# Kernel optimization log

Measured on AMD Instinct MI355X. Metric: run time of the kernel, lower is better.

Reference implementation:

```python
import jax, jax.numpy as jnp
import numpy as np

NU, NI = 100000, 50000
N = NU + NI
CU, CI = 100, 100
D = 64
NL = 3
NNZ = 4_000_000
CNNZ = 5000
B = 4096


def setup_inputs() -> dict:
    key = jax.random.key(0)
    ks = jax.random.split(key, 24)
    def edges(k1, k2, k3, nnz, n):
        return (jax.random.randint(k1, (nnz,), 0, n, dtype=jnp.int32),
                jax.random.randint(k2, (nnz,), 0, n, dtype=jnp.int32),
                jax.random.uniform(k3, (nnz,), dtype=jnp.float32) * 0.05)
    ar, ac, av = edges(ks[0], ks[1], ks[2], NNZ, N)
    s1r, s1c, s1v = edges(ks[3], ks[4], ks[5], NNZ, N)
    s2r, s2c, s2v = edges(ks[6], ks[7], ks[8], NNZ, N)
    cr, cc, cv = edges(ks[9], ks[10], ks[11], CNNZ, CU + CI)
    return {
        "user_emb": jax.random.normal(ks[12], (NU, D), dtype=jnp.float32) * 0.1,
        "item_emb": jax.random.normal(ks[13], (NI, D), dtype=jnp.float32) * 0.1,
        "adj_rows": ar, "adj_cols": ac, "adj_vals": av,
        "sg1_rows": s1r, "sg1_cols": s1c, "sg1_vals": s1v,
        "sg2_rows": s2r, "sg2_cols": s2c, "sg2_vals": s2v,
        "uc": jax.random.uniform(ks[14], (NU, CU), dtype=jnp.float32),
        "ic": jax.random.uniform(ks[15], (NI, CI), dtype=jnp.float32),
        "cg_rows": cr, "cg_cols": cc, "cg_vals": cv,
        "users": jax.random.randint(ks[16], (B,), 0, NU, dtype=jnp.int32),
        "items": jax.random.randint(ks[17], (B,), 0, NI, dtype=jnp.int32),
        "neg_items": jax.random.randint(ks[18], (B,), 0, NI, dtype=jnp.int32),
    }


def _gcn(rows, cols, vals, ego, n):
    """n_layers of SpMM propagation + mean over layer outputs (incl. layer 0)."""
    acc = ego
    x = ego
    for _ in range(NL):
        x = jax.ops.segment_sum(vals[:, None] * x[cols], rows, num_segments=n)
        acc = acc + x
    return acc / (NL + 1)


def reference(user_emb, item_emb,
              adj_rows, adj_cols, adj_vals,
              sg1_rows, sg1_cols, sg1_vals,
              sg2_rows, sg2_cols, sg2_vals,
              uc, ic, cg_rows, cg_cols, cg_vals,
              users, items, neg_items):
    ego = jnp.concatenate([user_emb, item_emb], axis=0)  # [N, D]
    e0 = _gcn(adj_rows, adj_cols, adj_vals, ego, N)
    e1 = _gcn(sg1_rows, sg1_cols, sg1_vals, ego, N)
    e2 = _gcn(sg2_rows, sg2_cols, sg2_vals, ego, N)
    # community GCN: project node embeddings onto community space, propagate, lift back
    ucf = uc.T @ user_emb                                # [CU, D]
    icf = ic.T @ item_emb                                # [CI, D]
    ec = _gcn(cg_rows, cg_cols, cg_vals,
              jnp.concatenate([ucf, icf], axis=0), CU + CI)
    u3 = uc @ ec[:CU]                                    # [NU, D]
    i3 = ic @ ec[CU:]                                    # [NI, D]
    user_f = jnp.concatenate([e0[:NU], e1[:NU], e2[:NU], u3], axis=1)  # [NU, 4D]
    item_f = jnp.concatenate([e0[NU:], e1[NU:], e2[NU:], i3], axis=1)  # [NI, 4D]
    ue = user_f[users]
    ie = item_f[items]
    ne = item_f[neg_items]
    # sup_logits = <u, i_pos> - <u, i_neg>
    return jnp.sum(ue * (ie - ne), axis=-1)
```

## Files before the change

kernel.cpp:

```cpp
#include <hip/hip_runtime.h>
#include <hip/hip_fp16.h>
#include <cstdint>
#include <cstddef>

#define NU_ 100000
#define NI_ 50000
#define NN_ 150000
#define D_  64
#define NNZ_ 4000000
#define CN_ 200
#define CNNZ_ 5000
#define B_ 4096

#define NB2   512
#define RPB2  293
#define SLICE 40
#define NBLK  512
#define ECAP  8448

#define PROJB 1024

#define VSC_   256.0f
#define IVSC_  (1.0f / 256.0f)

#if defined(__has_builtin)
#if __has_builtin(__builtin_amdgcn_cvt_scalef32_pk_f32_fp4) && \
    __has_builtin(__builtin_amdgcn_cvt_scalef32_pk_fp4_f32)
#define USE_FP4 1
#endif
#endif
#ifndef USE_FP4
#define USE_FP4 0
#endif

#if USE_FP4
#define FSC0 8.0f
#define FSC1 32.0f
#define FSC2 512.0f
#define ROWB 32
#else
#define FSC0 32.0f
#define FSC1 32.0f
#define FSC2 32.0f
#define ROWB 64
#endif

typedef float v2f __attribute__((ext_vector_type(2)));
typedef int   v4i __attribute__((ext_vector_type(4)));
typedef float v4f __attribute__((ext_vector_type(4)));

__device__ __forceinline__ float cv8(unsigned char b) {
    return __builtin_amdgcn_cvt_f32_fp8((int)b, 0);
}


#if USE_FP4
__global__ __launch_bounds__(256) void k_toq(const float* __restrict__ a,
                                             const float* __restrict__ b,
                                             unsigned* __restrict__ dst) {
    size_t gid = (size_t)blockIdx.x * 256 + threadIdx.x;
    size_t off = gid * 8;
    if (off >= (size_t)NN_ * D_) return;
    const float* src = (off < (size_t)NU_ * D_) ? a + off : b + (off - (size_t)NU_ * D_);
    float4 f0 = *(const float4*)src;
    float4 f1 = *(const float4*)(src + 4);
    unsigned w = 0;
    w = __builtin_amdgcn_cvt_scalef32_pk_fp4_f32(w, f0.x * FSC0, f0.y * FSC0, 1.0f, 0);
    w = __builtin_amdgcn_cvt_scalef32_pk_fp4_f32(w, f0.z * FSC0, f0.w * FSC0, 1.0f, 1);
    w = __builtin_amdgcn_cvt_scalef32_pk_fp4_f32(w, f1.x * FSC0, f1.y * FSC0, 1.0f, 2);
    w = __builtin_amdgcn_cvt_scalef32_pk_fp4_f32(w, f1.z * FSC0, f1.w * FSC0, 1.0f, 3);
    dst[gid] = w;
}
#else
__global__ __launch_bounds__(256) void k_toq(const float* __restrict__ a,
                                             const float* __restrict__ b,
                                             unsigned* __restrict__ dst) {
    size_t gid = (size_t)blockIdx.x * 256 + threadIdx.x;
    size_t off = gid * 4;
    if (off >= (size_t)NN_ * D_) return;
    const float* src = (off < (size_t)NU_ * D_) ? a + off : b + (off - (size_t)NU_ * D_);
    float4 f = *(const float4*)src;
    int p = 0;
    p = __builtin_amdgcn_cvt_pk_fp8_f32(f.x * FSC0, f.y * FSC0, p, false);
    p = __builtin_amdgcn_cvt_pk_fp8_f32(f.z * FSC0, f.w * FSC0, p, true);
    dst[gid] = (unsigned)p;
}
#endif


__global__ __launch_bounds__(256) void k_bin(const int* __restrict__ rows,
                                             const int* __restrict__ cols,
                                             const float* __restrict__ vals,
                                             int* __restrict__ bcnt,
                                             int2* __restrict__ gbuf) {
    __shared__ int lcur[NB2];
    int t = threadIdx.x;
    for (int i = t; i < NB2; i += 256) lcur[i] = 0;
    __syncthreads();
    size_t blockbase = (size_t)blockIdx.x * NB2 * SLICE;

    for (int base = blockIdx.x * 1024; base < NNZ_; base += gridDim.x * 1024) {
        int i0 = base + t * 4;
        if (i0 < NNZ_) {
            v4i r4 = __builtin_nontemporal_load((const v4i*)(rows + i0));
            v4i c4 = __builtin_nontemporal_load((const v4i*)(cols + i0));
            v4f v4 = __builtin_nontemporal_load((const v4f*)(vals + i0));
            #pragma unroll
            for (int k = 0; k < 4; k++) {
                int r = (k == 0) ? r4.x : (k == 1) ? r4.y : (k == 2) ? r4.z : r4.w;
                int c = (k == 0) ? c4.x : (k == 1) ? c4.y : (k == 2) ? c4.z : c4.w;
                float v = (k == 0) ? v4.x : (k == 1) ? v4.y : (k == 2) ? v4.z : v4.w;
                int b  = r / RPB2;
                int rl = r - b * RPB2;
                int pos = atomicAdd(&lcur[b], 1);
                if (pos < SLICE)
                    gbuf[blockbase + (size_t)b * SLICE + pos] =
                        make_int2((rl << 18) | c, __float_as_int(v));
            }
        }
    }
    __syncthreads();
    for (int i = t; i < NB2; i += 256)
        bcnt[(size_t)blockIdx.x * NB2 + i] = min(lcur[i], SLICE);
}


__global__ void k_btot(const int* __restrict__ bcnt, int* __restrict__ btot) {
    __shared__ int s[256];
    int b = blockIdx.x, t = threadIdx.x;
    int sum = 0;
    for (int sl = t; sl < NBLK; sl += 256) sum += bcnt[(size_t)sl * NB2 + b];
    s[t] = sum;
    __syncthreads();
    for (int o = 128; o > 0; o >>= 1) {
        if (t < o) s[t] += s[t + o];
        __syncthreads();
    }
    if (t == 0) btot[b] = s[0];
}

__global__ void k_bscan(const int* __restrict__ btot, int* __restrict__ bbase,
                        int* __restrict__ row_ptr) {
    __shared__ int s[NB2];
    int t = threadIdx.x;
    int v = btot[t];
    s[t] = v;
    __syncthreads();
    for (int o = 1; o < NB2; o <<= 1) {
        int x = (t >= o) ? s[t - o] : 0;
        __syncthreads();
        s[t] += x;
        __syncthreads();
    }
    bbase[t] = s[t] - v;
    if (t == NB2 - 1) row_ptr[NN_] = s[t];
}


__global__ __launch_bounds__(1024) void k_csr(const int* __restrict__ bcnt,
                                              const int2* __restrict__ gbuf,
                                              const int* __restrict__ bbase,
                                              const int* __restrict__ btot,
                                              int* __restrict__ row_ptr,
                                              unsigned* __restrict__ ep) {
    __shared__ int h[RPB2];
    __shared__ int hx[RPB2];
    __shared__ unsigned estage[ECAP];
    int b = blockIdx.x, t = threadIdx.x;
    for (int i = t; i < RPB2; i += 1024) h[i] = 0;
    __syncthreads();

    int sl = t >> 1, part = t & 1;
    int n = bcnt[(size_t)sl * NB2 + b];
    const int2* src = gbuf + ((size_t)sl * NB2 + b) * SLICE;

    for (int i = part; i < n; i += 2) {
        unsigned xv = *(const unsigned*)(src + i);
        atomicAdd(&h[xv >> 18], 1);
    }
    __syncthreads();

    if (t < RPB2) hx[t] = h[t];
    __syncthreads();
    for (int o = 1; o < RPB2; o <<= 1) {
        int x = 0;
        if (t < RPB2 && t >= o) x = hx[t - o];
        __syncthreads();
        if (t < RPB2) hx[t] += x;
        __syncthreads();
    }

    int base = bbase[b];
    int r0 = b * RPB2;
    if (t < RPB2) {
        int excl = hx[t] - h[t];
        if (r0 + t < NN_) row_ptr[r0 + t] = base + excl;
        h[t] = excl;
    }
    __syncthreads();

    for (int i = part; i < n; i += 2) {
        int2 e = src[i];
        unsigned ex = (unsigned)e.x;
        int rl = ex >> 18;
        unsigned c = ex & 0x3FFFFu;
        float v = __int_as_float(e.y) * VSC_;
        unsigned v8 = (unsigned)__builtin_amdgcn_cvt_pk_fp8_f32(v, 0.f, 0, false) & 0xFFu;
        int pos = atomicAdd(&h[rl], 1);
        if (pos < ECAP) estage[pos] = c | (v8 << 24);
    }
    __syncthreads();

    int total = btot[b];
    if (total > ECAP) total = ECAP;
    for (int i = t; i < total; i += 1024) ep[base + i] = estage[i];
}


__global__ __launch_bounds__(256) void k_spmm(const int* __restrict__ rp,
                                              const unsigned* __restrict__ ep,
                                              const unsigned char* __restrict__ xq,
                                              float invs, float outsc,
                                              unsigned char* __restrict__ xn) {
    int w = (blockIdx.x * 256 + threadIdx.x) >> 6;
    if (w >= NN_) return;
    int lane = threadIdx.x & 63;
    int oct = lane >> 3;
    int l8  = lane & 7;
    int j0 = rp[w], j1 = rp[w + 1];
    v2f a01 = {0.f, 0.f}, a23 = {0.f, 0.f}, a45 = {0.f, 0.f}, a67 = {0.f, 0.f};
    #pragma unroll 2
    for (int j = j0; j < j1; j += 8) {
        int je = j + oct;
        unsigned e = (je < j1) ? ep[je] : 0u;
        float v = __builtin_amdgcn_cvt_f32_fp8((int)e, 3) * invs;
        v2f vv = {v, v};
#if USE_FP4
        unsigned raw = *(const unsigned*)(xq + (size_t)(e & 0x3FFFFu) * 32 + l8 * 4);
        a01 += vv * __builtin_amdgcn_cvt_scalef32_pk_f32_fp4(raw, 1.0f, 0);
        a23 += vv * __builtin_amdgcn_cvt_scalef32_pk_f32_fp4(raw, 1.0f, 1);
        a45 += vv * __builtin_amdgcn_cvt_scalef32_pk_f32_fp4(raw, 1.0f, 2);
        a67 += vv * __builtin_amdgcn_cvt_scalef32_pk_f32_fp4(raw, 1.0f, 3);
#else
        uint2 raw = *(const uint2*)(xq + (size_t)(e & 0x3FFFFu) * 64 + l8 * 8);
        a01 += vv * __builtin_amdgcn_cvt_pk_f32_fp8((int)raw.x, false);
        a23 += vv * __builtin_amdgcn_cvt_pk_f32_fp8((int)raw.x, true);
        a45 += vv * __builtin_amdgcn_cvt_pk_f32_fp8((int)raw.y, false);
        a67 += vv * __builtin_amdgcn_cvt_pk_f32_fp8((int)raw.y, true);
#endif
    }
    float d0 = a01[0], d1 = a01[1], d2 = a23[0], d3 = a23[1];
    float d4 = a45[0], d5 = a45[1], d6 = a67[0], d7 = a67[1];
    #pragma unroll
    for (int o = 32; o >= 8; o >>= 1) {
        d0 += __shfl_xor(d0, o, 64); d1 += __shfl_xor(d1, o, 64);
        d2 += __shfl_xor(d2, o, 64); d3 += __shfl_xor(d3, o, 64);
        d4 += __shfl_xor(d4, o, 64); d5 += __shfl_xor(d5, o, 64);
        d6 += __shfl_xor(d6, o, 64); d7 += __shfl_xor(d7, o, 64);
    }
    if (lane < 8) {
#if USE_FP4
        unsigned o2 = 0;
        o2 = __builtin_amdgcn_cvt_scalef32_pk_fp4_f32(o2, d0 * outsc, d1 * outsc, 1.0f, 0);
        o2 = __builtin_amdgcn_cvt_scalef32_pk_fp4_f32(o2, d2 * outsc, d3 * outsc, 1.0f, 1);
        o2 = __builtin_amdgcn_cvt_scalef32_pk_fp4_f32(o2, d4 * outsc, d5 * outsc, 1.0f, 2);
        o2 = __builtin_amdgcn_cvt_scalef32_pk_fp4_f32(o2, d6 * outsc, d7 * outsc, 1.0f, 3);
        *(unsigned*)(xn + (size_t)w * 32 + l8 * 4) = o2;
#else
        int p0 = 0, p1 = 0;
        p0 = __builtin_amdgcn_cvt_pk_fp8_f32(d0 * outsc, d1 * outsc, p0, false);
        p0 = __builtin_amdgcn_cvt_pk_fp8_f32(d2 * outsc, d3 * outsc, p0, true);
        p1 = __builtin_amdgcn_cvt_pk_fp8_f32(d4 * outsc, d5 * outsc, p1, false);
        p1 = __builtin_amdgcn_cvt_pk_fp8_f32(d6 * outsc, d7 * outsc, p1, true);
        uint2 o2; o2.x = (unsigned)p0; o2.y = (unsigned)p1;
        *(uint2*)(xn + (size_t)w * 64 + l8 * 8) = o2;
#endif
    }
}


__global__ __launch_bounds__(256) void k_spmm_s(const int* __restrict__ rp,
                                                const unsigned* __restrict__ ep,
                                                const unsigned char* __restrict__ xq,
                                                float invs,
                                                const int* __restrict__ users,
                                                const int* __restrict__ items,
                                                const int* __restrict__ negs,
                                                float* __restrict__ x3s) {
    int s = (blockIdx.x * 256 + threadIdx.x) >> 6;
    if (s >= 3 * B_) return;
    int lane = threadIdx.x & 63;
    int oct = lane >> 3;
    int l8  = lane & 7;
    int node;
    if (s < B_)          node = users[s];
    else if (s < 2 * B_) node = NU_ + items[s - B_];
    else                 node = NU_ + negs[s - 2 * B_];
    int j0 = rp[node], j1 = rp[node + 1];
    v2f a01 = {0.f, 0.f}, a23 = {0.f, 0.f}, a45 = {0.f, 0.f}, a67 = {0.f, 0.f};
    #pragma unroll 2
    for (int j = j0; j < j1; j += 8) {
        int je = j + oct;
        unsigned e = (je < j1) ? ep[je] : 0u;
        float v = __builtin_amdgcn_cvt_f32_fp8((int)e, 3) * invs;
        v2f vv = {v, v};
#if USE_FP4
        unsigned raw = *(const unsigned*)(xq + (size_t)(e & 0x3FFFFu) * 32 + l8 * 4);
        a01 += vv * __builtin_amdgcn_cvt_scalef32_pk_f32_fp4(raw, 1.0f, 0);
        a23 += vv * __builtin_amdgcn_cvt_scalef32_pk_f32_fp4(raw, 1.0f, 1);
        a45 += vv * __builtin_amdgcn_cvt_scalef32_pk_f32_fp4(raw, 1.0f, 2);
        a67 += vv * __builtin_amdgcn_cvt_scalef32_pk_f32_fp4(raw, 1.0f, 3);
#else
        uint2 raw = *(const uint2*)(xq + (size_t)(e & 0x3FFFFu) * 64 + l8 * 8);
        a01 += vv * __builtin_amdgcn_cvt_pk_f32_fp8((int)raw.x, false);
        a23 += vv * __builtin_amdgcn_cvt_pk_f32_fp8((int)raw.x, true);
        a45 += vv * __builtin_amdgcn_cvt_pk_f32_fp8((int)raw.y, false);
        a67 += vv * __builtin_amdgcn_cvt_pk_f32_fp8((int)raw.y, true);
#endif
    }
    float d0 = a01[0], d1 = a01[1], d2 = a23[0], d3 = a23[1];
    float d4 = a45[0], d5 = a45[1], d6 = a67[0], d7 = a67[1];
    #pragma unroll
    for (int o = 32; o >= 8; o >>= 1) {
        d0 += __shfl_xor(d0, o, 64); d1 += __shfl_xor(d1, o, 64);
        d2 += __shfl_xor(d2, o, 64); d3 += __shfl_xor(d3, o, 64);
        d4 += __shfl_xor(d4, o, 64); d5 += __shfl_xor(d5, o, 64);
        d6 += __shfl_xor(d6, o, 64); d7 += __shfl_xor(d7, o, 64);
    }
    if (lane < 8) {
        float* dst = x3s + (size_t)s * D_ + l8 * 8;
        *(float4*)dst       = make_float4(d0, d1, d2, d3);
        *(float4*)(dst + 4) = make_float4(d4, d5, d6, d7);
    }
}


__device__ __forceinline__ float ldq(const unsigned char* x, size_t row, int lane, float inv) {
#if USE_FP4
    unsigned byte = x[row * 32 + (lane >> 1)];
    v2f pr = __builtin_amdgcn_cvt_scalef32_pk_f32_fp4(byte, 1.0f, 0);
    return ((lane & 1) ? pr[1] : pr[0]) * inv;
#else
    return cv8(x[row * 64 + lane]) * inv;
#endif
}

template<bool FIRST>
__global__ void k_dot_graph(const float* __restrict__ ue, const float* __restrict__ ie,
                            const unsigned char* __restrict__ x1,
                            const unsigned char* __restrict__ x2,
                            const float* __restrict__ x3s,
                            const int* __restrict__ users, const int* __restrict__ items,
                            const int* __restrict__ negs, float* __restrict__ out) {
    int w = (blockIdx.x * blockDim.x + threadIdx.x) >> 6;
    int lane = threadIdx.x & 63;
    if (w >= B_) return;
    int u = users[w], ip = items[w], in_ = negs[w];
    const float i1 = 1.0f / FSC1, i2 = 1.0f / FSC2;
    size_t ru = (size_t)u, ri = (size_t)(NU_ + ip), rn = (size_t)(NU_ + in_);
    float du = ue[(size_t)u * D_ + lane]
             + ldq(x1, ru, lane, i1) + ldq(x2, ru, lane, i2) + x3s[(size_t)w * D_ + lane];
    float di = ie[(size_t)ip * D_ + lane]
             + ldq(x1, ri, lane, i1) + ldq(x2, ri, lane, i2) + x3s[(size_t)(B_ + w) * D_ + lane];
    float dn = ie[(size_t)in_ * D_ + lane]
             + ldq(x1, rn, lane, i1) + ldq(x2, rn, lane, i2) + x3s[(size_t)(2 * B_ + w) * D_ + lane];
    float p = du * (di - dn);
    for (int o = 32; o > 0; o >>= 1) p += __shfl_xor(p, o, 64);
    if (lane == 0) {
        if (FIRST) out[w] = p * 0.0625f;
        else       out[w] += p * 0.0625f;
    }
}


__global__ __launch_bounds__(256) void k_proj(const float* __restrict__ mat,
                                              const float* __restrict__ emb,
                                              int n, float* __restrict__ pbuf) {
    __shared__ float se[8 * 64];
    __shared__ float sc[8 * 100];
    int t = threadIdx.x;
    int d = t & 63, c0 = t >> 6;
    float a[25];
    #pragma unroll
    for (int k = 0; k < 25; k++) a[k] = 0.f;

    int upb = (n + gridDim.x - 1) / gridDim.x;
    int u0 = blockIdx.x * upb;
    int u1 = min(u0 + upb, n);
    int ub = u0;
    for (; ub + 8 <= u1; ub += 8) {
        const float4* e4 = (const float4*)(emb + (size_t)ub * 64);
        const float4* c4 = (const float4*)(mat + (size_t)ub * 100);
        float4* se4 = (float4*)se;
        float4* sc4 = (float4*)sc;
        for (int idx = t; idx < 328; idx += 256) {
            if (idx < 128) se4[idx] = e4[idx];
            else           sc4[idx - 128] = c4[idx - 128];
        }
        __syncthreads();
        #pragma unroll
        for (int ul = 0; ul < 8; ++ul) {
            float ev = se[(ul << 6) + d];
            #pragma unroll
            for (int k = 0; k < 25; k++)
                a[k] += sc[ul * 100 + c0 + (k << 2)] * ev;
        }
        __syncthreads();
    }
    if (ub < u1) {
        int m = u1 - ub;
        for (int idx = t; idx < m * 64; idx += 256) se[idx] = emb[(size_t)ub * 64 + idx];
        for (int idx = t; idx < m * 100; idx += 256) sc[idx] = mat[(size_t)ub * 100 + idx];
        __syncthreads();
        for (int ul = 0; ul < m; ++ul) {
            float ev = se[(ul << 6) + d];
            #pragma unroll
            for (int k = 0; k < 25; k++)
                a[k] += sc[ul * 100 + c0 + (k << 2)] * ev;
        }
    }
    float* dst = pbuf + (size_t)blockIdx.x * 6400;
    #pragma unroll
    for (int k = 0; k < 25; k++)
        dst[t + (k << 8)] = a[k];
}

__global__ __launch_bounds__(256) void k_preduce(const float* __restrict__ pbuf,
                                                 float* __restrict__ dst) {
    int e = blockIdx.x * 256 + threadIdx.x;
    const float* src = pbuf + (size_t)blockIdx.y * 128 * 6400 + e;
    float s = 0.f;
    #pragma unroll 8
    for (int p = 0; p < 128; p++) s += src[(size_t)p * 6400];
    atomicAdd(&dst[e], s);
}


__global__ void k_cspmm(const int* __restrict__ r, const int* __restrict__ c,
                        const float* __restrict__ v, const float* __restrict__ x,
                        float* __restrict__ xn) {
    int w = (blockIdx.x * blockDim.x + threadIdx.x) >> 6;
    int lane = threadIdx.x & 63;
    if (w >= CNNZ_) return;
    int rr = r[w], cc = c[w];
    float vv = v[w];
    atomicAdd(&xn[rr * 64 + lane], vv * x[cc * 64 + lane]);
}


__global__ void k_dot_comm(const float* __restrict__ uc, const float* __restrict__ ic,
                           const float* __restrict__ cego, const float* __restrict__ cb1,
                           const float* __restrict__ cb2, const float* __restrict__ cb3,
                           const int* __restrict__ users, const int* __restrict__ items,
                           const int* __restrict__ negs, float* __restrict__ out) {
    int w = (blockIdx.x * blockDim.x + threadIdx.x) >> 6;
    int lane = threadIdx.x & 63;
    if (w >= B_) return;
    int u = users[w], ip = items[w], in_ = negs[w];
    float u3 = 0.f, i3p = 0.f, i3n = 0.f;
    for (int cc = 0; cc < 100; ++cc) {
        int eu = cc * 64 + lane, ei = (100 + cc) * 64 + lane;
        float evU = cego[eu] + cb1[eu] + cb2[eu] + cb3[eu];
        float evI = cego[ei] + cb1[ei] + cb2[ei] + cb3[ei];
        u3  += uc[(size_t)u * 100 + cc] * evU;
        i3p += ic[(size_t)ip * 100 + cc] * evI;
        i3n += ic[(size_t)in_ * 100 + cc] * evI;
    }
    float p = u3 * (i3p - i3n);
    for (int o = 32; o > 0; o >>= 1) p += __shfl_xor(p, o, 64);
    if (lane == 0) out[w] += p * 0.0625f;
}


static inline char* alignp(char*& p, size_t bytes) {
    char* r = p;
    p += (bytes + 255) & ~(size_t)255;
    return r;
}

extern "C" void kernel_launch(void* const* d_in, const int* in_sizes, int n_in,
                              void* d_out, int out_size, void* d_ws, size_t ws_size,
                              hipStream_t stream) {
    const float* uemb = (const float*)d_in[0];
    const float* iemb = (const float*)d_in[1];
    const float* uc   = (const float*)d_in[11];
    const float* ic   = (const float*)d_in[12];
    const int*   cgr  = (const int*)d_in[13];
    const int*   cgc  = (const int*)d_in[14];
    const float* cgv  = (const float*)d_in[15];
    const int*   users = (const int*)d_in[16];
    const int*   items = (const int*)d_in[17];
    const int*   negs  = (const int*)d_in[18];
    float* out = (float*)d_out;

    char* p = (char*)d_ws;
    char*  A      = alignp(p, (size_t)NBLK * NB2 * SLICE * 8);
    unsigned char* egoq = (unsigned char*)alignp(p, (size_t)NN_ * 64);
    unsigned* ep  = (unsigned*)alignp(p, (size_t)NNZ_ * 4);
    float* x3s    = (float*)alignp(p, (size_t)3 * B_ * D_ * 4);
    int*   row_ptr= (int*)  alignp(p, (size_t)(NN_ + 1) * 4);
    int*   bcnt   = (int*)  alignp(p, (size_t)NBLK * NB2 * 4);
    int*   btot   = (int*)  alignp(p, NB2 * 4);
    int*   bbase  = (int*)  alignp(p, NB2 * 4);
    float* cego   = (float*)alignp(p, (size_t)CN_ * D_ * 4);
    float* cbs    = (float*)alignp(p, (size_t)3 * CN_ * D_ * 4);
    float* cb1 = cbs, *cb2 = cbs + CN_ * D_, *cb3 = cbs + 2 * CN_ * D_;

    int2*          gbuf = (int2*)A;
    unsigned char* xq1  = (unsigned char*)A;
    unsigned char* xq2  = (unsigned char*)(A + (size_t)NN_ * ROWB);
    float*         pbuf = (float*)A;

    const int gSp = (NN_ * 64) / 256;
    const int gS3 = (3 * B_ * 64) / 256;
    const int gB  = (B_ * 64) / 256;
    const int gC  = (CNNZ_ * 64) / 256;
#if USE_FP4
    const int gTQ = (NN_ * D_ / 8 + 255) / 256;
#else
    const int gTQ = (NN_ * D_ / 4 + 255) / 256;
#endif

    k_toq<<<gTQ, 256, 0, stream>>>(uemb, iemb, (unsigned*)egoq);

    const float inv1 = 1.0f / (256.0f * FSC0);
    const float inv2 = 1.0f / (256.0f * FSC1);
    const float inv3 = 1.0f / (256.0f * FSC2);

    for (int g = 0; g < 3; ++g) {
        const int*   rows = (const int*)d_in[2 + g * 3];
        const int*   cols = (const int*)d_in[3 + g * 3];
        const float* vals = (const float*)d_in[4 + g * 3];

        k_bin  <<<NBLK, 256, 0, stream>>>(rows, cols, vals, bcnt, gbuf);
        k_btot <<<NB2, 256, 0, stream>>>(bcnt, btot);
        k_bscan<<<1, NB2, 0, stream>>>(btot, bbase, row_ptr);
        k_csr  <<<NB2, 1024, 0, stream>>>(bcnt, gbuf, bbase, btot, row_ptr, ep);

        k_spmm<<<gSp, 256, 0, stream>>>(row_ptr, ep, egoq, inv1, FSC1, xq1);
        k_spmm<<<gSp, 256, 0, stream>>>(row_ptr, ep, xq1,  inv2, FSC2, xq2);
        k_spmm_s<<<gS3, 256, 0, stream>>>(row_ptr, ep, xq2, inv3, users, items, negs, x3s);

        if (g == 0)
            k_dot_graph<true ><<<gB, 256, 0, stream>>>(uemb, iemb, xq1, xq2, x3s,
                                                       users, items, negs, out);
        else
            k_dot_graph<false><<<gB, 256, 0, stream>>>(uemb, iemb, xq1, xq2, x3s,
                                                       users, items, negs, out);
    }

    hipMemsetAsync(cego, 0, (size_t)CN_ * D_ * 4, stream);
    k_proj<<<PROJB, 256, 0, stream>>>(uc, uemb, NU_, pbuf);
    k_preduce<<<dim3(25, 8), 256, 0, stream>>>(pbuf, cego);
    k_proj<<<PROJB, 256, 0, stream>>>(ic, iemb, NI_, pbuf);
    k_preduce<<<dim3(25, 8), 256, 0, stream>>>(pbuf, cego + 100 * 64);

    hipMemsetAsync(cbs, 0, (size_t)3 * CN_ * D_ * 4, stream);
    k_cspmm<<<gC, 256, 0, stream>>>(cgr, cgc, cgv, cego, cb1);
    k_cspmm<<<gC, 256, 0, stream>>>(cgr, cgc, cgv, cb1, cb2);
    k_cspmm<<<gC, 256, 0, stream>>>(cgr, cgc, cgv, cb2, cb3);

    k_dot_comm<<<gB, 256, 0, stream>>>(uc, ic, cego, cb1, cb2, cb3,
                                       users, items, negs, out);
}
```

Measured before the change: 879.8 us.

## Sort CSR edges within each row by column panel and fold SpMM scales

```diff
diff --git a/kernel.cpp b/kernel.cpp
--- a/kernel.cpp
+++ b/kernel.cpp
@@ -18,10 +18,13 @@
 #define NBLK  512
 #define ECAP  8448
 
+#define NP    4
+#define COLP  37500
+#define HSZ   (RPB2 * NP)
+
 #define PROJB 1024
 
 #define VSC_   256.0f
-#define IVSC_  (1.0f / 256.0f)
 
 #if defined(__has_builtin)
 #if __has_builtin(__builtin_amdgcn_cvt_scalef32_pk_f32_fp4) && \
@@ -163,11 +166,12 @@
                                               const int* __restrict__ btot,
                                               int* __restrict__ row_ptr,
                                               unsigned* __restrict__ ep) {
-    __shared__ int h[RPB2];
-    __shared__ int hx[RPB2];
+    __shared__ int h[HSZ];
+    __shared__ int hx[HSZ];
+    __shared__ int aux[1024];
     __shared__ unsigned estage[ECAP];
     int b = blockIdx.x, t = threadIdx.x;
-    for (int i = t; i < RPB2; i += 1024) h[i] = 0;
+    for (int i = t; i < HSZ; i += 1024) h[i] = 0;
     __syncthreads();
 
     int sl = t >> 1, part = t & 1;
@@ -176,27 +180,31 @@
 
     for (int i = part; i < n; i += 2) {
         unsigned xv = *(const unsigned*)(src + i);
-        atomicAdd(&h[xv >> 18], 1);
-    }
-    __syncthreads();
-
-    if (t < RPB2) hx[t] = h[t];
-    __syncthreads();
-    for (int o = 1; o < RPB2; o <<= 1) {
-        int x = 0;
-        if (t < RPB2 && t >= o) x = hx[t - o];
-        __syncthreads();
-        if (t < RPB2) hx[t] += x;
-        __syncthreads();
-    }
+        int rl = xv >> 18;
+        int pnl = (int)(xv & 0x3FFFFu) / COLP;
+        atomicAdd(&h[rl * NP + pnl], 1);
+    }
+    __syncthreads();
+
+    int a0 = (2 * t     < HSZ) ? h[2 * t]     : 0;
+    int a1 = (2 * t + 1 < HSZ) ? h[2 * t + 1] : 0;
+    aux[t] = a0 + a1;
+    __syncthreads();
+    for (int o = 1; o < 1024; o <<= 1) {
+        int x = (t >= o) ? aux[t - o] : 0;
+        __syncthreads();
+        aux[t] += x;
+        __syncthreads();
+    }
+    int excl = t ? aux[t - 1] : 0;
+    if (2 * t     < HSZ) hx[2 * t]     = excl;
+    if (2 * t + 1 < HSZ) hx[2 * t + 1] = excl + a0;
+    __syncthreads();
 
     int base = bbase[b];
     int r0 = b * RPB2;
-    if (t < RPB2) {
-        int excl = hx[t] - h[t];
-        if (r0 + t < NN_) row_ptr[r0 + t] = base + excl;
-        h[t] = excl;
-    }
+    int rows_b = min(RPB2, NN_ - r0);
+    for (int i = t; i < rows_b; i += 1024) row_ptr[r0 + i] = base + hx[i * NP];
     __syncthreads();
 
     for (int i = part; i < n; i += 2) {
@@ -204,9 +212,10 @@
         unsigned ex = (unsigned)e.x;
         int rl = ex >> 18;
         unsigned c = ex & 0x3FFFFu;
+        int pnl = (int)c / COLP;
         float v = __int_as_float(e.y) * VSC_;
         unsigned v8 = (unsigned)__builtin_amdgcn_cvt_pk_fp8_f32(v, 0.f, 0, false) & 0xFFu;
-        int pos = atomicAdd(&h[rl], 1);
+        int pos = atomicAdd(&hx[rl * NP + pnl], 1);
         if (pos < ECAP) estage[pos] = c | (v8 << 24);
     }
     __syncthreads();
@@ -220,7 +229,7 @@
 __global__ __launch_bounds__(256) void k_spmm(const int* __restrict__ rp,
                                               const unsigned* __restrict__ ep,
                                               const unsigned char* __restrict__ xq,
-                                              float invs, float outsc,
+                                              float finsc,
                                               unsigned char* __restrict__ xn) {
     int w = (blockIdx.x * 256 + threadIdx.x) >> 6;
     if (w >= NN_) return;
@@ -233,7 +242,7 @@
     for (int j = j0; j < j1; j += 8) {
         int je = j + oct;
         unsigned e = (je < j1) ? ep[je] : 0u;
-        float v = __builtin_amdgcn_cvt_f32_fp8((int)e, 3) * invs;
+        float v = __builtin_amdgcn_cvt_f32_fp8((int)e, 3);
         v2f vv = {v, v};
 #if USE_FP4
         unsigned raw = *(const unsigned*)(xq + (size_t)(e & 0x3FFFFu) * 32 + l8 * 4);
@@ -261,17 +270,17 @@
     if (lane < 8) {
 #if USE_FP4
         unsigned o2 = 0;
-        o2 = __builtin_amdgcn_cvt_scalef32_pk_fp4_f32(o2, d0 * outsc, d1 * outsc, 1.0f, 0);
-        o2 = __builtin_amdgcn_cvt_scalef32_pk_fp4_f32(o2, d2 * outsc, d3 * outsc, 1.0f, 1);
-        o2 = __builtin_amdgcn_cvt_scalef32_pk_fp4_f32(o2, d4 * outsc, d5 * outsc, 1.0f, 2);
-        o2 = __builtin_amdgcn_cvt_scalef32_pk_fp4_f32(o2, d6 * outsc, d7 * outsc, 1.0f, 3);
+        o2 = __builtin_amdgcn_cvt_scalef32_pk_fp4_f32(o2, d0 * finsc, d1 * finsc, 1.0f, 0);
+        o2 = __builtin_amdgcn_cvt_scalef32_pk_fp4_f32(o2, d2 * finsc, d3 * finsc, 1.0f, 1);
+        o2 = __builtin_amdgcn_cvt_scalef32_pk_fp4_f32(o2, d4 * finsc, d5 * finsc, 1.0f, 2);
+        o2 = __builtin_amdgcn_cvt_scalef32_pk_fp4_f32(o2, d6 * finsc, d7 * finsc, 1.0f, 3);
         *(unsigned*)(xn + (size_t)w * 32 + l8 * 4) = o2;
 #else
         int p0 = 0, p1 = 0;
-        p0 = __builtin_amdgcn_cvt_pk_fp8_f32(d0 * outsc, d1 * outsc, p0, false);
-        p0 = __builtin_amdgcn_cvt_pk_fp8_f32(d2 * outsc, d3 * outsc, p0, true);
-        p1 = __builtin_amdgcn_cvt_pk_fp8_f32(d4 * outsc, d5 * outsc, p1, false);
-        p1 = __builtin_amdgcn_cvt_pk_fp8_f32(d6 * outsc, d7 * outsc, p1, true);
+        p0 = __builtin_amdgcn_cvt_pk_fp8_f32(d0 * finsc, d1 * finsc, p0, false);
+        p0 = __builtin_amdgcn_cvt_pk_fp8_f32(d2 * finsc, d3 * finsc, p0, true);
+        p1 = __builtin_amdgcn_cvt_pk_fp8_f32(d4 * finsc, d5 * finsc, p1, false);
+        p1 = __builtin_amdgcn_cvt_pk_fp8_f32(d6 * finsc, d7 * finsc, p1, true);
         uint2 o2; o2.x = (unsigned)p0; o2.y = (unsigned)p1;
         *(uint2*)(xn + (size_t)w * 64 + l8 * 8) = o2;
 #endif
@@ -282,7 +291,7 @@
 __global__ __launch_bounds__(256) void k_spmm_s(const int* __restrict__ rp,
                                                 const unsigned* __restrict__ ep,
                                                 const unsigned char* __restrict__ xq,
-                                                float invs,
+                                                float finsc,
                                                 const int* __restrict__ users,
                                                 const int* __restrict__ items,
                                                 const int* __restrict__ negs,
@@ -302,7 +311,7 @@
     for (int j = j0; j < j1; j += 8) {
         int je = j + oct;
         unsigned e = (je < j1) ? ep[je] : 0u;
-        float v = __builtin_amdgcn_cvt_f32_fp8((int)e, 3) * invs;
+        float v = __builtin_amdgcn_cvt_f32_fp8((int)e, 3);
         v2f vv = {v, v};
 #if USE_FP4
         unsigned raw = *(const unsigned*)(xq + (size_t)(e & 0x3FFFFu) * 32 + l8 * 4);
@@ -329,8 +338,8 @@
     }
     if (lane < 8) {
         float* dst = x3s + (size_t)s * D_ + l8 * 8;
-        *(float4*)dst       = make_float4(d0, d1, d2, d3);
-        *(float4*)(dst + 4) = make_float4(d4, d5, d6, d7);
+        *(float4*)dst       = make_float4(d0 * finsc, d1 * finsc, d2 * finsc, d3 * finsc);
+        *(float4*)(dst + 4) = make_float4(d4 * finsc, d5 * finsc, d6 * finsc, d7 * finsc);
     }
 }
 
@@ -523,9 +532,9 @@
 
     k_toq<<<gTQ, 256, 0, stream>>>(uemb, iemb, (unsigned*)egoq);
 
-    const float inv1 = 1.0f / (256.0f * FSC0);
-    const float inv2 = 1.0f / (256.0f * FSC1);
-    const float inv3 = 1.0f / (256.0f * FSC2);
+    const float fin1 = FSC1 / (256.0f * FSC0);
+    const float fin2 = FSC2 / (256.0f * FSC1);
+    const float fin3 = 1.0f / (256.0f * FSC2);
 
     for (int g = 0; g < 3; ++g) {
         const int*   rows = (const int*)d_in[2 + g * 3];
@@ -537,9 +546,9 @@
         k_bscan<<<1, NB2, 0, stream>>>(btot, bbase, row_ptr);
         k_csr  <<<NB2, 1024, 0, stream>>>(bcnt, gbuf, bbase, btot, row_ptr, ep);
 
-        k_spmm<<<gSp, 256, 0, stream>>>(row_ptr, ep, egoq, inv1, FSC1, xq1);
-        k_spmm<<<gSp, 256, 0, stream>>>(row_ptr, ep, xq1,  inv2, FSC2, xq2);
-        k_spmm_s<<<gS3, 256, 0, stream>>>(row_ptr, ep, xq2, inv3, users, items, negs, x3s);
+        k_spmm<<<gSp, 256, 0, stream>>>(row_ptr, ep, egoq, fin1, xq1);
+        k_spmm<<<gSp, 256, 0, stream>>>(row_ptr, ep, xq1,  fin2, xq2);
+        k_spmm_s<<<gS3, 256, 0, stream>>>(row_ptr, ep, xq2, fin3, users, items, negs, x3s);
 
         if (g == 0)
             k_dot_graph<true ><<<gB, 256, 0, stream>>>(uemb, iemb, xq1, xq2, x3s,
```

After: 881.2 us. Within noise of the previous version (+0.2%).
